# Performance work log

Hardware: AMD Instinct MI355X
Metric: run time of the kernel (lower is better)

Reference implementation:

```python
import jax, jax.numpy as jnp
import numpy as np

B, T, D = 16, 2000, 512
L_ORDER, R_ORDER = 10, 5
L_STRIDE, R_STRIDE = 2, 2
KERNEL_RES = True


def setup_inputs() -> dict:
    key = jax.random.key(0)
    k1, k2 = jax.random.split(key)
    inputs = jax.random.normal(k1, (B, T, D), dtype=jnp.float32)
    filt = jax.random.normal(k2, (L_ORDER + R_ORDER + 1, D), dtype=jnp.float32)
    return {"inputs": inputs, "filt": filt}


def reference(inputs, filt):
    # FSMN memory block: strided dilated depthwise conv over time.
    # inputs: (B, T, D); filt: (l_order + r_order + 1, D)
    batch, frames, dims = inputs.shape
    L = L_ORDER * L_STRIDE  # left zero-pad
    R = R_ORDER * R_STRIDE  # right zero-pad
    x = jnp.pad(inputs, ((0, 0), (L, R), (0, 0)))

    # center tap
    out = inputs * filt[L_ORDER]
    # left taps: tap k sits at (frame - (l_order - k) * l_stride) in the
    # unpadded signal -> offset k*l_stride in the padded signal.
    for k in range(L_ORDER):
        off = k * L_STRIDE
        out = out + x[:, off:off + frames] * filt[k]
    # right taps: tap k sits at frame + 1 + k*r_stride -> padded offset L+1+k*r_stride.
    for k in range(R_ORDER):
        off = L + 1 + k * R_STRIDE
        out = out + x[:, off:off + frames] * filt[L_ORDER + 1 + k]

    if KERNEL_RES:
        out = out + inputs
    return out
```

## Files before the change

### kernel.cpp

```cpp
#include <hip/hip_runtime.h>
#include <hip/hip_bf16.h>


typedef float f32x4 __attribute__((ext_vector_type(4)));
typedef __attribute__((address_space(1))) const unsigned int gas_u32;
typedef __attribute__((address_space(3))) unsigned int las_u32;

constexpr int B = 16;
constexpr int T = 2000;
constexpr int D = 512;
constexpr int DH = 256;
constexpr int NTAP = 16;
constexpr int S = 10;
constexpr int NSTRIP = T / S;
constexpr int WROWS = 39;
constexpr int NXCD = 8;

__global__ __launch_bounds__(256) void fsmn_lds_kernel(
    const float* __restrict__ x,
    const float* __restrict__ filt,
    float* __restrict__ out)
{
    __shared__ float smem[WROWS * DH];

    const int nbl = B * 2 * NSTRIP;
    const int cpx = nbl / NXCD;
    int bid = blockIdx.x;
    bid = (bid & (NXCD - 1)) * cpx + (bid >> 3);

    const int strip = bid % NSTRIP;
    const int bh    = bid / NSTRIP;
    const int dhalf = bh & 1;
    const int b     = bh >> 1;
    const int t0    = strip * S;

    const int tid  = (int)threadIdx.x;
    const int wave = tid >> 6;
    const int lane = tid & 63;

    const float* gx = x + (size_t)(b * T) * D + dhalf * DH;
#pragma unroll
    for (int j = 0; j < 10; ++j) {
        const int m = wave + 4 * j;
        if (m < WROWS) {
            const int p = t0 - 20 + m;
            if (p >= 0 && p < T) {
                const float* src = gx + (size_t)p * D + lane * 4;
                __builtin_amdgcn_global_load_lds(
                    (gas_u32*)src,
                    (las_u32*)&smem[m * DH],
                    16, 0, 0);
            } else {
                ((f32x4*)&smem[m * DH])[lane] = (f32x4)(0.0f);
            }
        }
    }

    const int c = tid;
    float F[NTAP];
#pragma unroll
    for (int k = 0; k < NTAP; ++k) F[k] = filt[k * D + dhalf * DH + c];
    F[10] += 1.0f;

    __syncthreads();

    float W[WROWS];
#pragma unroll
    for (int m = 0; m < WROWS; ++m) W[m] = smem[m * DH + c];

    float* op = out + (size_t)(b * T + t0) * D + dhalf * DH + c;
#pragma unroll
    for (int i = 0; i < S; ++i) {
        float a = W[i + 20] * F[10];
#pragma unroll
        for (int k = 0; k < 10; ++k) a = fmaf(W[i + 2 * k], F[k], a);
#pragma unroll
        for (int k = 0; k < 5; ++k)  a = fmaf(W[i + 21 + 2 * k], F[11 + k], a);
        __builtin_nontemporal_store(a, &op[(size_t)i * D]);
    }
}

extern "C" void kernel_launch(void* const* d_in, const int* in_sizes, int n_in,
                              void* d_out, int out_size, void* d_ws, size_t ws_size,
                              hipStream_t stream) {
    const float* x    = (const float*)d_in[0];
    const float* filt = (const float*)d_in[1];
    float* out        = (float*)d_out;

    const int grid = B * 2 * NSTRIP;
    fsmn_lds_kernel<<<grid, 256, 0, stream>>>(x, filt, out);
}
```

Measured before the change: 27.84 us.

## Retile FSMN kernel to 64-channel, 20-row strips split across waves

```diff
diff --git a/kernel.cpp b/kernel.cpp
--- a/kernel.cpp
+++ b/kernel.cpp
@@ -2,81 +2,84 @@
 #include <hip/hip_bf16.h>
 
 
-typedef float f32x4 __attribute__((ext_vector_type(4)));
 typedef __attribute__((address_space(1))) const unsigned int gas_u32;
 typedef __attribute__((address_space(3))) unsigned int las_u32;
 
 constexpr int B = 16;
 constexpr int T = 2000;
 constexpr int D = 512;
-constexpr int DH = 256;
+constexpr int DH = 64;
+constexpr int NDG = D / DH;
 constexpr int NTAP = 16;
-constexpr int S = 10;
+constexpr int S = 20;
 constexpr int NSTRIP = T / S;
-constexpr int WROWS = 39;
+constexpr int WROWS = S + 29;
 constexpr int NXCD = 8;
 
-__global__ __launch_bounds__(256) void fsmn_lds_kernel(
+__global__ __launch_bounds__(256, 6) void fsmn_lds_kernel(
     const float* __restrict__ x,
     const float* __restrict__ filt,
     float* __restrict__ out)
 {
     __shared__ float smem[WROWS * DH];
 
-    const int nbl = B * 2 * NSTRIP;
+    const int nbl = B * NDG * NSTRIP;
     const int cpx = nbl / NXCD;
     int bid = blockIdx.x;
     bid = (bid & (NXCD - 1)) * cpx + (bid >> 3);
 
     const int strip = bid % NSTRIP;
-    const int bh    = bid / NSTRIP;
-    const int dhalf = bh & 1;
-    const int b     = bh >> 1;
+    const int rest  = bid / NSTRIP;
+    const int dgrp  = rest & (NDG - 1);
+    const int b     = rest >> 3;
     const int t0    = strip * S;
+    const int d0    = dgrp * DH;
 
     const int tid  = (int)threadIdx.x;
     const int wave = tid >> 6;
     const int lane = tid & 63;
 
-    const float* gx = x + (size_t)(b * T) * D + dhalf * DH;
+    const float* gx = x + (size_t)(b * T) * D + d0;
 #pragma unroll
-    for (int j = 0; j < 10; ++j) {
+    for (int j = 0; j < 13; ++j) {
         const int m = wave + 4 * j;
         if (m < WROWS) {
             const int p = t0 - 20 + m;
             if (p >= 0 && p < T) {
-                const float* src = gx + (size_t)p * D + lane * 4;
+                const float* src = gx + (size_t)p * D + lane;
                 __builtin_amdgcn_global_load_lds(
                     (gas_u32*)src,
                     (las_u32*)&smem[m * DH],
-                    16, 0, 0);
+                    4, 0, 0);
             } else {
-                ((f32x4*)&smem[m * DH])[lane] = (f32x4)(0.0f);
+                smem[m * DH + lane] = 0.0f;
             }
         }
     }
 
-    const int c = tid;
+    const int c   = tid & (DH - 1);
+    const int grp = tid >> 6;
     float F[NTAP];
 #pragma unroll
-    for (int k = 0; k < NTAP; ++k) F[k] = filt[k * D + dhalf * DH + c];
+    for (int k = 0; k < NTAP; ++k) F[k] = filt[k * D + d0 + c];
     F[10] += 1.0f;
 
     __syncthreads();
 
-    float W[WROWS];
+    const int i0 = grp * 5;
+    float W[34];
 #pragma unroll
-    for (int m = 0; m < WROWS; ++m) W[m] = smem[m * DH + c];
+    for (int r = 0; r < 34; ++r) W[r] = smem[(i0 + r) * DH + c];
 
-    float* op = out + (size_t)(b * T + t0) * D + dhalf * DH + c;
+    float* op = out + (size_t)(b * T + t0 + i0) * D + d0 + c;
 #pragma unroll
-    for (int i = 0; i < S; ++i) {
-        float a = W[i + 20] * F[10];
+    for (int j = 0; j < 5; ++j) {
+        float a = W[j + 20] * F[10];
 #pragma unroll
-        for (int k = 0; k < 10; ++k) a = fmaf(W[i + 2 * k], F[k], a);
+        for (int k = 0; k < 10; ++k) a = fmaf(W[j + 2 * k], F[k], a);
 #pragma unroll
-        for (int k = 0; k < 5; ++k)  a = fmaf(W[i + 21 + 2 * k], F[11 + k], a);
-        __builtin_nontemporal_store(a, &op[(size_t)i * D]);
+        for (int k = 0; k < 5; ++k)  a = fmaf(W[j + 21 + 2 * k], F[11 + k], a);
+        __builtin_nontemporal_store(a, &op[(size_t)j * D]);
     }
 }
 
@@ -87,6 +90,6 @@
     const float* filt = (const float*)d_in[1];
     float* out        = (float*)d_out;
 
-    const int grid = B * 2 * NSTRIP;
+    const int grid = B * NDG * NSTRIP;
     fsmn_lds_kernel<<<grid, 256, 0, stream>>>(x, filt, out);
 }
```

New measurement: 30.17 us. 8.4% more time.
